# Performance work log

Measured on AMD Instinct MI355X. Metric: run time of the kernel, lower is better.

The kernel has to match this reference:

```python
import jax, jax.numpy as jnp
import numpy as np

# ---- MjCambrianEyeConfig constants ----
RES = (128, 128)              # sensor resolution (pixels)
SENSOR = (0.01, 0.01)         # sensor size Lx, Ly (meters)
APERTURE_OPEN = 0.5           # fraction of max aperture
FOCAL = 0.05                  # propagation distance z2 = config.focal[0] (meters)
WAVELENGTHS = (610e-9, 530e-9, 470e-9)  # R, G, B (meters)


def _rs_prop(u1, z, FX, FY, lmbda):
    # Rayleigh-Sommerfeld transfer-function propagation.
    k = 2.0 * np.pi / lmbda
    arg = 1.0 - (lmbda * FX) ** 2 - (lmbda * FY) ** 2  # (My, Mx)
    valid = jnp.sqrt(FX ** 2 + FY ** 2) < 1.0 / lmbda   # matches H_valid; arg>0 <=> valid
    H = jnp.where(valid, jnp.exp(1j * (k * z) * jnp.sqrt(jnp.where(arg > 0, arg, 0.0))), 0.0)
    U1 = jnp.fft.fft2(jnp.fft.fftshift(u1))
    U2 = jnp.fft.fftshift(H) * U1
    return jnp.fft.ifftshift(jnp.fft.ifft2(U2))


def _simple_psf(depth):
    Mx, My = RES[0] * 2, RES[1] * 2
    if Mx % 2 == 0:
        Mx += 1
    if My % 2 == 0:
        My += 1
    Lx, Ly = SENSOR
    dx, dy = Lx / Mx, Ly / My
    x1 = jnp.linspace(-Lx / 2.0, Lx / 2.0, Mx)
    y1 = jnp.linspace(-Ly / 2.0, Ly / 2.0, My)
    X1, Y1 = jnp.meshgrid(x1, y1)                         # (My, Mx)
    fx = jnp.linspace(-1.0 / (2.0 * dx), 1.0 / (2.0 * dx), Mx)
    fy = jnp.linspace(-1.0 / (2.0 * dy), 1.0 / (2.0 * dy), My)
    FX, FY = jnp.meshgrid(fx, fy)
    ap_radius = float(np.clip(APERTURE_OPEN, 0.0, 1.0)) * dx * (Mx // 2)
    R2 = X1 ** 2 + Y1 ** 2
    A = (jnp.sqrt(R2) / (ap_radius + 1e-7) <= 1.0).astype(jnp.float32)  # aperture mask
    z1 = jnp.mean(depth)
    psfs = []
    for lam in WAVELENGTHS:  # small fixed loop over 3 wavelengths
        k = 2.0 * np.pi / lam
        u = jnp.exp(1j * k * jnp.sqrt(R2 + z1 ** 2)) * A  # spherical wave at aperture
        u = _rs_prop(u, FOCAL, FX, FY, lam)
        psf = jnp.abs(u) ** 2
        psfs.append(psf / (jnp.sum(psf) + 1e-7))
    return jnp.stack(psfs, axis=-1).astype(jnp.float32)  # (My, Mx, 3)


def setup_inputs() -> dict:
    key = jax.random.key(0)
    k1, k2 = jax.random.split(key)
    image = jax.random.uniform(k1, (128, 128, 3), dtype=jnp.float32)
    depth = jax.random.uniform(k2, (128, 128), dtype=jnp.float32)
    return {"image": image, "depth": depth}


def reference(image, depth):
    psf = _simple_psf(depth)                       # (My, Mx, 3)
    lhs = jnp.transpose(image, (2, 0, 1))[None]    # (1, 3, H, W)
    rhs = jnp.transpose(psf, (2, 0, 1))[:, None]   # (3, 1, Kh, Kw)
    # Per-channel 'same' cross-correlation == torch conv2d per channel
    out = jax.lax.conv_general_dilated(lhs, rhs, window_strides=(1, 1), padding='SAME', feature_group_count=3)
    img = jnp.transpose(out[0], (1, 2, 0))         # (H, W, 3)
    return img, psf
```

## Files before the change

kernel.cpp:

```cpp
#include <hip/hip_runtime.h>
#include <math.h>

#define NN 257
#define NN2 66049
#define PROW 260
#define PCH (PROW * NN)
#define NRZ 17
#define FSW 288

#define SWG(f) (((((f) >> 2) ^ (((f) >> 5) & 7)) << 2))
#define SW(f) (SWG(f) | ((f) & 3))

static const double D_PI = 3.14159265358979323846;

__device__ __forceinline__ double lam_of(int c) {
    return c == 0 ? 610e-9 : (c == 1 ? 530e-9 : 470e-9);
}

__device__ __forceinline__ float2 phase_of(double rev) {
    rev -= floor(rev);
    float ang = (float)(2.0 * D_PI * rev);
    float sv, cv;
    __sincosf(ang, &sv, &cv);
    return make_float2(cv, sv);
}

__global__ __launch_bounds__(256) void k_prep(const float* __restrict__ depth, const float* __restrict__ img,
                                              double* zs, float* __restrict__ imgp, float2* __restrict__ twg) {
    if (blockIdx.x == 0) {
        __shared__ double s[256];
        double acc = 0.0;
        for (int i = threadIdx.x; i < 16384; i += 256) acc += (double)depth[i];
        s[threadIdx.x] = acc;
        __syncthreads();
        for (int o = 128; o > 0; o >>= 1) {
            if (threadIdx.x < o) s[threadIdx.x] += s[threadIdx.x + o];
            __syncthreads();
        }
        if (threadIdx.x == 0) {
            zs[0] = s[0] / 16384.0;
            zs[1] = 0.0; zs[2] = 0.0; zs[3] = 0.0;
        }
    } else if (blockIdx.x == 193) {
        int m = threadIdx.x;
        double th = 2.0 * D_PI * (double)m / 257.0;
        double sv, cv; sincos(th, &sv, &cv);
        twg[m] = make_float2((float)cv, (float)(-sv));
        if (m == 0) {
            th = 2.0 * D_PI * 256.0 / 257.0;
            sincos(th, &sv, &cv);
            twg[256] = make_float2((float)cv, (float)(-sv));
        }
    } else {
        int idx = (blockIdx.x - 1) * 256 + threadIdx.x;
        int c = idx / 16384;
        int r = idx & 16383;
        imgp[c * 16384 + r] = img[r * 3 + c];
    }
}

template <int SIGN, int MODE>
__global__ __launch_bounds__(256) void k_dft(const float2* __restrict__ in, float2* __restrict__ out,
                                             const float2* __restrict__ twg, const double* __restrict__ zs,
                                             float* __restrict__ raw, double* __restrict__ sums) {
    __shared__ float4 col[NN];
    __shared__ float2 twL[NN];
    __shared__ float4 sacc2[3][64][2];
    __shared__ float4 red[4];
    const int ah = blockIdx.x;
    const int by = blockIdx.y;
    const int c = blockIdx.z;
    int bc0, bc1;
    if (MODE == 0 || MODE == 3) {
        bc0 = (by < 64) ? 2 * by : 256;
        bc1 = (by < 64) ? bc0 + 1 : 256;
    } else if (MODE == 1) {
        bc0 = (by < 64) ? 2 * by : 128;
        bc1 = (by < 64) ? bc0 + 1 : 128;
    } else {
        bc0 = 2 * by;
        bc1 = (bc0 < 256) ? bc0 + 1 : 256;
    }
    const float dupf = (bc1 == bc0) ? 0.f : 1.f;
    const int tid = threadIdx.x;

    for (int t = tid; t < NN; t += 256) {
        twL[t] = twg[t];
        float2 v0, v1;
        if (MODE == 0) {
            int js = t + 129; if (js >= NN) js -= NN;
            const double step = 0.01 / 256.0;
            double yy = -0.005 + js * step;
            double z1 = zs[0];
            double lam = lam_of(c);
            const double ap = 0.5 * (0.01 / 257.0) * 128.0 + 1e-7;
            {
                int is = bc0 + 129; if (is >= NN) is -= NN;
                double x = -0.005 + is * step;
                double r2 = x * x + yy * yy;
                v0 = make_float2(0.f, 0.f);
                if (sqrt(r2) <= ap) v0 = phase_of(sqrt(r2 + z1 * z1) / lam);
            }
            {
                int is = bc1 + 129; if (is >= NN) is -= NN;
                double x = -0.005 + is * step;
                double r2 = x * x + yy * yy;
                v1 = make_float2(0.f, 0.f);
                if (sqrt(r2) <= ap) v1 = phase_of(sqrt(r2 + z1 * z1) / lam);
            }
        } else {
            v0 = in[(c * NN + t) * NN + bc0];
            v1 = in[(c * NN + t) * NN + bc1];
            if (MODE == 2) {
                int ps = t + 129; if (ps >= NN) ps -= NN;
                const double fstep = 25700.0 / 256.0;
                double fy = -12850.0 + ps * fstep;
                double lam = lam_of(c);
                double ilam2 = 1.0 / (lam * lam);
                double kzr = 0.05 / lam;
                {
                    int qs = bc0 + 129; if (qs >= NN) qs -= NN;
                    double fx = -12850.0 + qs * fstep;
                    double lfx = lam * fx, lfy = lam * fy;
                    double a2 = 1.0 - lfx * lfx - lfy * lfy;
                    float2 hh = make_float2(0.f, 0.f);
                    if (fx * fx + fy * fy < ilam2) hh = phase_of(kzr * sqrt(a2 > 0.0 ? a2 : 0.0));
                    v0 = make_float2(v0.x * hh.x - v0.y * hh.y, v0.x * hh.y + v0.y * hh.x);
                }
                {
                    int qs = bc1 + 129; if (qs >= NN) qs -= NN;
                    double fx = -12850.0 + qs * fstep;
                    double lfx = lam * fx, lfy = lam * fy;
                    double a2 = 1.0 - lfx * lfx - lfy * lfy;
                    float2 hh = make_float2(0.f, 0.f);
                    if (fx * fx + fy * fy < ilam2) hh = phase_of(kzr * sqrt(a2 > 0.0 ? a2 : 0.0));
                    v1 = make_float2(v1.x * hh.x - v1.y * hh.y, v1.x * hh.y + v1.y * hh.x);
                }
            }
        }
        col[t] = make_float4(v0.x, v0.y, v1.x, v1.y);
    }
    __syncthreads();

    const float invn4 = (float)(1.0 / ((double)NN2 * (double)NN2));
    const int q = tid >> 6;
    const int al = tid & 63;
    int aval[2];
    aval[0] = ah * 128 + al;
    aval[1] = aval[0] + 64;

    float cx[2][4], cy[2][4], wx[2], wy[2];
    #pragma unroll
    for (int aa = 0; aa < 2; ++aa) {
        #pragma unroll
        for (int m = 0; m < 4; ++m) {
            int sm = (aval[aa] * (q + 4 * m)) % 257;
            float2 tt = twL[sm];
            cx[aa][m] = tt.x; cy[aa][m] = -SIGN * tt.y;
        }
        float2 w16 = twL[(16 * aval[aa]) % 257];
        wx[aa] = w16.x; wy[aa] = -SIGN * w16.y;
    }

    float AX0[2] = {0.f, 0.f}, AY0[2] = {0.f, 0.f}, BX0[2] = {0.f, 0.f}, BY0[2] = {0.f, 0.f};
    float AX1[2] = {0.f, 0.f}, AY1[2] = {0.f, 0.f}, BX1[2] = {0.f, 0.f}, BY1[2] = {0.f, 0.f};

    for (int j = 0; j < 16; ++j) {
        const int tbase = q + 16 * j;
        #pragma unroll
        for (int m = 0; m < 4; ++m) {
            float4 v = col[tbase + 4 * m];
            #pragma unroll
            for (int aa = 0; aa < 2; ++aa) {
                float cxr = cx[aa][m], cyr = cy[aa][m];
                if (m < 2) {
                    AX0[aa] = fmaf(v.x, cxr, AX0[aa]); AX0[aa] = fmaf(-v.y, cyr, AX0[aa]);
                    AY0[aa] = fmaf(v.x, cyr, AY0[aa]); AY0[aa] = fmaf(v.y, cxr, AY0[aa]);
                    BX0[aa] = fmaf(v.z, cxr, BX0[aa]); BX0[aa] = fmaf(-v.w, cyr, BX0[aa]);
                    BY0[aa] = fmaf(v.z, cyr, BY0[aa]); BY0[aa] = fmaf(v.w, cxr, BY0[aa]);
                } else {
                    AX1[aa] = fmaf(v.x, cxr, AX1[aa]); AX1[aa] = fmaf(-v.y, cyr, AX1[aa]);
                    AY1[aa] = fmaf(v.x, cyr, AY1[aa]); AY1[aa] = fmaf(v.y, cxr, AY1[aa]);
                    BX1[aa] = fmaf(v.z, cxr, BX1[aa]); BX1[aa] = fmaf(-v.w, cyr, BX1[aa]);
                    BY1[aa] = fmaf(v.z, cyr, BY1[aa]); BY1[aa] = fmaf(v.w, cxr, BY1[aa]);
                }
                float nx = fmaf(cxr, wx[aa], -cyr * wy[aa]);
                float ny = fmaf(cxr, wy[aa], cyr * wx[aa]);
                cx[aa][m] = nx; cy[aa][m] = ny;
            }
        }
    }

    float ax0[2], ay0[2], ax1[2], ay1[2];
    #pragma unroll
    for (int aa = 0; aa < 2; ++aa) {
        ax0[aa] = AX0[aa] + AX1[aa]; ay0[aa] = AY0[aa] + AY1[aa];
        ax1[aa] = BX0[aa] + BX1[aa]; ay1[aa] = BY0[aa] + BY1[aa];
    }

    if (q == 0) {
        float4 v = col[256];
        #pragma unroll
        for (int aa = 0; aa < 2; ++aa) {
            float2 tb = twL[aval[aa]];
            float ex = tb.x, ey = SIGN * tb.y;
            ax0[aa] = fmaf(v.x, ex, ax0[aa]); ax0[aa] = fmaf(-v.y, ey, ax0[aa]);
            ay0[aa] = fmaf(v.x, ey, ay0[aa]); ay0[aa] = fmaf(v.y, ex, ay0[aa]);
            ax1[aa] = fmaf(v.z, ex, ax1[aa]); ax1[aa] = fmaf(-v.w, ey, ax1[aa]);
            ay1[aa] = fmaf(v.z, ey, ay1[aa]); ay1[aa] = fmaf(v.w, ex, ay1[aa]);
        }
    } else {
        #pragma unroll
        for (int aa = 0; aa < 2; ++aa)
            sacc2[q - 1][al][aa] = make_float4(ax0[aa], ay0[aa], ax1[aa], ay1[aa]);
    }
    __syncthreads();

    const bool mv0 = (MODE == 0) ? (bc0 <= 127) : (bc0 >= 1 && bc0 <= 128);
    const bool mv1 = ((MODE == 0) ? (bc1 <= 127) : (bc1 >= 1 && bc1 <= 128)) && (bc1 != bc0);
    const int bm0 = (MODE == 0) ? (255 - bc0) : (257 - bc0);
    const int bm1 = (MODE == 0) ? (255 - bc1) : (257 - bc1);
    const bool pm = (MODE == 3) && (bc0 <= 127);

    double sum_local = 0.0;
    if (q == 0) {
        #pragma unroll
        for (int aa = 0; aa < 2; ++aa) {
            #pragma unroll
            for (int r = 0; r < 3; ++r) {
                float4 b = sacc2[r][al][aa];
                ax0[aa] += b.x; ay0[aa] += b.y; ax1[aa] += b.z; ay1[aa] += b.w;
            }
            if (MODE < 3) {
                out[(c * NN + bc0) * NN + aval[aa]] = make_float2(ax0[aa], ay0[aa]);
                out[(c * NN + bc1) * NN + aval[aa]] = make_float2(ax1[aa], ay1[aa]);
                if (MODE < 2) {
                    const int a = aval[aa];
                    const int am = (a == 0) ? 0 : (257 - a);
                    if (mv0) {
                        int m = 2 * a + ((MODE == 1) ? 2 * bc0 : 0);
                        m %= 257;
                        float fx = twL[m].x, fy = -SIGN * twL[m].y;
                        out[(c * NN + bm0) * NN + am] =
                            make_float2(ax0[aa] * fx - ay0[aa] * fy, ax0[aa] * fy + ay0[aa] * fx);
                    }
                    if (mv1) {
                        int m = 2 * a + ((MODE == 1) ? 2 * bc1 : 0);
                        m %= 257;
                        float fx = twL[m].x, fy = -SIGN * twL[m].y;
                        out[(c * NN + bm1) * NN + am] =
                            make_float2(ax1[aa] * fx - ay1[aa] * fy, ax1[aa] * fy + ay1[aa] * fx);
                    }
                }
            } else {
                int jj0 = bc0 + 129; if (jj0 >= NN) jj0 -= NN;
                int jj1 = bc1 + 129; if (jj1 >= NN) jj1 -= NN;
                int ii = aval[aa] + 129; if (ii >= NN) ii -= NN;
                float m0 = fmaf(ax0[aa], ax0[aa], ay0[aa] * ay0[aa]) * invn4;
                float m1 = fmaf(ax1[aa], ax1[aa], ay1[aa] * ay1[aa]) * invn4;
                raw[c * PCH + jj0 * PROW + ii] = m0;
                raw[c * PCH + jj1 * PROW + ii] = m1;
                sum_local += (double)m0 + (double)(dupf * m1);
                if (pm) {
                    int im = 256 - ii;
                    raw[c * PCH + (256 - jj0) * PROW + im] = m0;
                    raw[c * PCH + (256 - jj1) * PROW + im] = m1;
                    sum_local += (double)m0 + (double)(dupf * m1);
                }
            }
        }
    }

    if (ah == (int)gridDim.x - 1) {
        float c_ = twL[tid].x, s_ = SIGN * twL[tid].y;
        float4 cv = col[tid];
        float tx0 = cv.x * c_ - cv.y * s_;
        float ty0 = cv.x * s_ + cv.y * c_;
        float tx1 = cv.z * c_ - cv.w * s_;
        float ty1 = cv.z * s_ + cv.w * c_;
        if (tid == 0) {
            c_ = twL[256].x; s_ = SIGN * twL[256].y;
            cv = col[256];
            tx0 += cv.x * c_ - cv.y * s_;
            ty0 += cv.x * s_ + cv.y * c_;
            tx1 += cv.z * c_ - cv.w * s_;
            ty1 += cv.z * s_ + cv.w * c_;
        }
        for (int o = 32; o > 0; o >>= 1) {
            tx0 += __shfl_down(tx0, o);
            ty0 += __shfl_down(ty0, o);
            tx1 += __shfl_down(tx1, o);
            ty1 += __shfl_down(ty1, o);
        }
        int wid = tid >> 6;
        if ((tid & 63) == 0) red[wid] = make_float4(tx0, ty0, tx1, ty1);
        __syncthreads();
        if (tid == 0) {
            float Xx0 = red[0].x + red[1].x + red[2].x + red[3].x;
            float Xy0 = red[0].y + red[1].y + red[2].y + red[3].y;
            float Xx1 = red[0].z + red[1].z + red[2].z + red[3].z;
            float Xy1 = red[0].w + red[1].w + red[2].w + red[3].w;
            if (MODE < 3) {
                out[(c * NN + bc0) * NN + 256] = make_float2(Xx0, Xy0);
                out[(c * NN + bc1) * NN + 256] = make_float2(Xx1, Xy1);
                if (MODE < 2) {
                    if (mv0) {
                        int m = 512 + ((MODE == 1) ? 2 * bc0 : 0);
                        m %= 257;
                        float fx = twL[m].x, fy = -SIGN * twL[m].y;
                        out[(c * NN + bm0) * NN + 1] = make_float2(Xx0 * fx - Xy0 * fy, Xx0 * fy + Xy0 * fx);
                    }
                    if (mv1) {
                        int m = 512 + ((MODE == 1) ? 2 * bc1 : 0);
                        m %= 257;
                        float fx = twL[m].x, fy = -SIGN * twL[m].y;
                        out[(c * NN + bm1) * NN + 1] = make_float2(Xx1 * fx - Xy1 * fy, Xx1 * fy + Xy1 * fx);
                    }
                }
            } else {
                int jj0 = bc0 + 129; if (jj0 >= NN) jj0 -= NN;
                int jj1 = bc1 + 129; if (jj1 >= NN) jj1 -= NN;
                float m0 = fmaf(Xx0, Xx0, Xy0 * Xy0) * invn4;
                float m1 = fmaf(Xx1, Xx1, Xy1 * Xy1) * invn4;
                raw[c * PCH + jj0 * PROW + 128] = m0;
                raw[c * PCH + jj1 * PROW + 128] = m1;
                sum_local += (double)m0 + (double)(dupf * m1);
                if (pm) {
                    raw[c * PCH + (256 - jj0) * PROW + 128] = m0;
                    raw[c * PCH + (256 - jj1) * PROW + 128] = m1;
                    sum_local += (double)m0 + (double)(dupf * m1);
                }
            }
        }
    }

    if (MODE == 3) {
        if (tid < 64) {
            double s = sum_local;
            for (int o = 32; o > 0; o >>= 1) s += __shfl_down(s, o);
            if (tid == 0) atomicAdd(&sums[c], s);
        }
    }
}

#define CM16(A, P, Q, iv)                                                                                   \
    A.x = fmaf(iv.x, Q.x, A.x); A.x = fmaf(iv.y, P.w, A.x); A.x = fmaf(iv.z, P.z, A.x); A.x = fmaf(iv.w, P.y, A.x); \
    A.y = fmaf(iv.x, Q.y, A.y); A.y = fmaf(iv.y, Q.x, A.y); A.y = fmaf(iv.z, P.w, A.y); A.y = fmaf(iv.w, P.z, A.y); \
    A.z = fmaf(iv.x, Q.z, A.z); A.z = fmaf(iv.y, Q.y, A.z); A.z = fmaf(iv.z, Q.x, A.z); A.z = fmaf(iv.w, P.w, A.z); \
    A.w = fmaf(iv.x, Q.w, A.w); A.w = fmaf(iv.y, Q.z, A.w); A.w = fmaf(iv.z, Q.y, A.w); A.w = fmaf(iv.w, Q.x, A.w);

__global__ __launch_bounds__(256) void k_conv(const float* __restrict__ imgp, const float* __restrict__ psf,
                                              float* __restrict__ part) {
    __shared__ float F[8][FSW];
    __shared__ float simg[15][132];
    __shared__ float sacc[3][4][260];
    const int yt = blockIdx.x;
    const int rz = blockIdx.y;
    const int c = blockIdx.z;
    const int y0 = yt * 8;
    const int r0 = 121 - y0 + 8 * rz;
    const int tid = threadIdx.x;
    const int tx = tid & 7;
    const int ty = (tid >> 3) & 7;
    const int rh = tid >> 6;
    const int x0 = 16 * tx;
    const int ulo = 8 * rz - 7;

    for (int g = tid; g < 8 * 65; g += 256) {
        int rr = g / 65, q = g - 65 * rr;
        const float* G = psf + c * PCH + (r0 + rr) * PROW + 4 * q;
        float4 A = *(const float4*)G;
        if (q < 64) {
            F[rr][SW(256 - 4 * q)] = A.x;
            F[rr][SW(255 - 4 * q)] = A.y;
            F[rr][SW(254 - 4 * q)] = A.z;
            F[rr][SW(253 - 4 * q)] = A.w;
        } else {
            F[rr][SW(0)] = A.x;
        }
    }
    for (int g = tid; g < 15 * 32; g += 256) {
        int rw = g >> 5, q = g & 31;
        int u = ulo + rw;
        float4 v = make_float4(0.f, 0.f, 0.f, 0.f);
        if (u >= 0 && u < 128) v = *(const float4*)(imgp + c * 16384 + u * 128 + 4 * q);
        *(float4*)&simg[rw][4 * q] = v;
    }
    __syncthreads();

    float4 A0 = make_float4(0.f, 0.f, 0.f, 0.f), A1 = A0, A2 = A0, A3 = A0;

    #pragma unroll
    for (int rr2 = 0; rr2 < 2; ++rr2) {
        const int rr = 2 * rh + rr2;
        const float* Fr = &F[rr][0];
        const float* I = &simg[ty + rr][0];
        float4 W0c = *(const float4*)(Fr + SWG(x0 + 128));
        float4 W1c = *(const float4*)(Fr + SWG(x0 + 132));
        float4 W2c = *(const float4*)(Fr + SWG(x0 + 136));
        float4 W3c = *(const float4*)(Fr + SWG(x0 + 140));
        #pragma unroll 2
        for (int vb = 0; vb < 128; vb += 4) {
            float4 Wm1 = *(const float4*)(Fr + SWG(x0 + 124 - vb));
            float4 iv = *(const float4*)(I + vb);
            CM16(A0, Wm1, W0c, iv)
            CM16(A1, W0c, W1c, iv)
            CM16(A2, W1c, W2c, iv)
            CM16(A3, W2c, W3c, iv)
            W3c = W2c; W2c = W1c; W1c = W0c; W0c = Wm1;
        }
    }

    if (rh != 0) {
        int s = tid & 63;
        *(float4*)&sacc[rh - 1][0][4 * s] = A0;
        *(float4*)&sacc[rh - 1][1][4 * s] = A1;
        *(float4*)&sacc[rh - 1][2][4 * s] = A2;
        *(float4*)&sacc[rh - 1][3][4 * s] = A3;
    }
    __syncthreads();
    if (rh == 0) {
        int s = tid;
        #pragma unroll
        for (int r = 0; r < 3; ++r) {
            float4 b0 = *(const float4*)&sacc[r][0][4 * s];
            float4 b1 = *(const float4*)&sacc[r][1][4 * s];
            float4 b2 = *(const float4*)&sacc[r][2][4 * s];
            float4 b3 = *(const float4*)&sacc[r][3][4 * s];
            A0.x += b0.x; A0.y += b0.y; A0.z += b0.z; A0.w += b0.w;
            A1.x += b1.x; A1.y += b1.y; A1.z += b1.z; A1.w += b1.w;
            A2.x += b2.x; A2.y += b2.y; A2.z += b2.z; A2.w += b2.w;
            A3.x += b3.x; A3.y += b3.y; A3.z += b3.z; A3.w += b3.w;
        }
        const int y = y0 + ty;
        float* dst = part + ((rz * 3 + c) * 128 + y) * 128 + x0;
        *(float4*)dst = A0;
        *(float4*)(dst + 4) = A1;
        *(float4*)(dst + 8) = A2;
        *(float4*)(dst + 12) = A3;
    }
}

__global__ __launch_bounds__(256) void k_final(const float* __restrict__ part, const float* __restrict__ raw,
                                               const double* __restrict__ zs, float* __restrict__ out) {
    int gid = blockIdx.x * 256 + threadIdx.x;
    if (gid < 49152) {
        int c = gid >> 14;
        int r = gid & 16383;
        float s = 0.f;
        #pragma unroll
        for (int rz = 0; rz < NRZ; ++rz) s += part[((rz * 3 + c) * 128 + (r >> 7)) * 128 + (r & 127)];
        float inv = (float)(1.0 / (zs[1 + c] + 1e-7));
        out[r * 3 + c] = s * inv;
    } else {
        int o = gid - 49152;
        if (o < 3 * NN2) {
            int idx = o / 3, c = o - 3 * idx;
            int j = idx / NN, i = idx - NN * j;
            float inv = (float)(1.0 / (zs[1 + c] + 1e-7));
            out[49152 + o] = raw[c * PCH + j * PROW + i] * inv;
        }
    }
}

extern "C" void kernel_launch(void* const* d_in, const int* in_sizes, int n_in,
                              void* d_out, int out_size, void* d_ws, size_t ws_size,
                              hipStream_t stream) {
    const float* img = (const float*)d_in[0];
    const float* depth = (const float*)d_in[1];
    float* out = (float*)d_out;

    char* ws = (char*)d_ws;
    double* zs = (double*)ws;
    float2* bufA = (float2*)(ws + 64);
    float2* bufB = bufA + 3 * NN2;
    float* raw = (float*)(bufB + 3 * NN2);
    float* imgp = raw + 3 * PCH;
    float2* twg = (float2*)(imgp + 3 * 16384);
    float* part = (float*)((char*)twg + 2176);

    k_prep<<<194, 256, 0, stream>>>(depth, img, zs, imgp, twg);
    k_dft<-1, 0><<<dim3(2, 65, 3), 256, 0, stream>>>(nullptr, bufA, twg, zs, nullptr, nullptr);
    k_dft<-1, 1><<<dim3(2, 65, 3), 256, 0, stream>>>(bufA, bufB, twg, zs, nullptr, nullptr);
    k_dft< 1, 2><<<dim3(1, 129, 3), 256, 0, stream>>>(bufB, bufA, twg, zs, nullptr, nullptr);
    k_dft< 1, 3><<<dim3(2, 65, 3), 256, 0, stream>>>(bufA, nullptr, twg, zs, raw, zs + 1);
    k_conv<<<dim3(16, NRZ, 3), 256, 0, stream>>>(imgp, raw, part);
    k_final<<<(49152 + 3 * NN2 + 255) / 256, 256, 0, stream>>>(part, raw, zs, out);
}
```

Baseline: 85.52 us.

## Fold prep kernel into DFT and conv kernels, remove one launch

Removes the separate prep kernel. Each DFT block now computes the twiddle table in-block with double-precision sincos. Every MODE 0 block recomputes the depth mean with its own reduction, and the first MODE 2 block zeroes the sum accumulators. The conv kernel reads the interleaved image directly with strided loads instead of using a pre-transposed planar copy. This saves one kernel launch and a small memory pass, at the cost of redundant depth reductions across 390 blocks and per-block sincos work.

```diff
diff --git a/kernel.cpp b/kernel.cpp
--- a/kernel.cpp
+++ b/kernel.cpp
@@ -25,43 +25,9 @@
     return make_float2(cv, sv);
 }
 
-__global__ __launch_bounds__(256) void k_prep(const float* __restrict__ depth, const float* __restrict__ img,
-                                              double* zs, float* __restrict__ imgp, float2* __restrict__ twg) {
-    if (blockIdx.x == 0) {
-        __shared__ double s[256];
-        double acc = 0.0;
-        for (int i = threadIdx.x; i < 16384; i += 256) acc += (double)depth[i];
-        s[threadIdx.x] = acc;
-        __syncthreads();
-        for (int o = 128; o > 0; o >>= 1) {
-            if (threadIdx.x < o) s[threadIdx.x] += s[threadIdx.x + o];
-            __syncthreads();
-        }
-        if (threadIdx.x == 0) {
-            zs[0] = s[0] / 16384.0;
-            zs[1] = 0.0; zs[2] = 0.0; zs[3] = 0.0;
-        }
-    } else if (blockIdx.x == 193) {
-        int m = threadIdx.x;
-        double th = 2.0 * D_PI * (double)m / 257.0;
-        double sv, cv; sincos(th, &sv, &cv);
-        twg[m] = make_float2((float)cv, (float)(-sv));
-        if (m == 0) {
-            th = 2.0 * D_PI * 256.0 / 257.0;
-            sincos(th, &sv, &cv);
-            twg[256] = make_float2((float)cv, (float)(-sv));
-        }
-    } else {
-        int idx = (blockIdx.x - 1) * 256 + threadIdx.x;
-        int c = idx / 16384;
-        int r = idx & 16383;
-        imgp[c * 16384 + r] = img[r * 3 + c];
-    }
-}
-
 template <int SIGN, int MODE>
 __global__ __launch_bounds__(256) void k_dft(const float2* __restrict__ in, float2* __restrict__ out,
-                                             const float2* __restrict__ twg, const double* __restrict__ zs,
+                                             const float* __restrict__ depth,
                                              float* __restrict__ raw, double* __restrict__ sums) {
     __shared__ float4 col[NN];
     __shared__ float2 twL[NN];
@@ -84,14 +50,37 @@
     const float dupf = (bc1 == bc0) ? 0.f : 1.f;
     const int tid = threadIdx.x;
 
+    if (MODE == 2) {
+        if (ah == 0 && by == 0 && tid == 0) sums[c] = 0.0;
+    }
+
     for (int t = tid; t < NN; t += 256) {
-        twL[t] = twg[t];
+        double th = 2.0 * D_PI * (double)t / 257.0;
+        double sv, cv; sincos(th, &sv, &cv);
+        twL[t] = make_float2((float)cv, (float)(-sv));
+    }
+
+    double z1 = 0.0;
+    if (MODE == 0) {
+        double* sred = (double*)sacc2;
+        double acc = 0.0;
+        for (int i = tid; i < 16384; i += 256) acc += (double)depth[i];
+        sred[tid] = acc;
+        __syncthreads();
+        for (int o = 128; o > 0; o >>= 1) {
+            if (tid < o) sred[tid] += sred[tid + o];
+            __syncthreads();
+        }
+        z1 = sred[0] / 16384.0;
+        __syncthreads();
+    }
+
+    for (int t = tid; t < NN; t += 256) {
         float2 v0, v1;
         if (MODE == 0) {
             int js = t + 129; if (js >= NN) js -= NN;
             const double step = 0.01 / 256.0;
             double yy = -0.005 + js * step;
-            double z1 = zs[0];
             double lam = lam_of(c);
             const double ap = 0.5 * (0.01 / 257.0) * 128.0 + 1e-7;
             {
@@ -349,7 +338,7 @@
     A.z = fmaf(iv.x, Q.z, A.z); A.z = fmaf(iv.y, Q.y, A.z); A.z = fmaf(iv.z, Q.x, A.z); A.z = fmaf(iv.w, P.w, A.z); \
     A.w = fmaf(iv.x, Q.w, A.w); A.w = fmaf(iv.y, Q.z, A.w); A.w = fmaf(iv.z, Q.y, A.w); A.w = fmaf(iv.w, Q.x, A.w);
 
-__global__ __launch_bounds__(256) void k_conv(const float* __restrict__ imgp, const float* __restrict__ psf,
+__global__ __launch_bounds__(256) void k_conv(const float* __restrict__ img, const float* __restrict__ psf,
                                               float* __restrict__ part) {
     __shared__ float F[8][FSW];
     __shared__ float simg[15][132];
@@ -383,7 +372,10 @@
         int rw = g >> 5, q = g & 31;
         int u = ulo + rw;
         float4 v = make_float4(0.f, 0.f, 0.f, 0.f);
-        if (u >= 0 && u < 128) v = *(const float4*)(imgp + c * 16384 + u * 128 + 4 * q);
+        if (u >= 0 && u < 128) {
+            const float* I = img + (u * 128 + 4 * q) * 3 + c;
+            v = make_float4(I[0], I[3], I[6], I[9]);
+        }
         *(float4*)&simg[rw][4 * q] = v;
     }
     __syncthreads();
@@ -442,7 +434,7 @@
 }
 
 __global__ __launch_bounds__(256) void k_final(const float* __restrict__ part, const float* __restrict__ raw,
-                                               const double* __restrict__ zs, float* __restrict__ out) {
+                                               const double* __restrict__ sums, float* __restrict__ out) {
     int gid = blockIdx.x * 256 + threadIdx.x;
     if (gid < 49152) {
         int c = gid >> 14;
@@ -450,14 +442,14 @@
         float s = 0.f;
         #pragma unroll
         for (int rz = 0; rz < NRZ; ++rz) s += part[((rz * 3 + c) * 128 + (r >> 7)) * 128 + (r & 127)];
-        float inv = (float)(1.0 / (zs[1 + c] + 1e-7));
+        float inv = (float)(1.0 / (sums[c] + 1e-7));
         out[r * 3 + c] = s * inv;
     } else {
         int o = gid - 49152;
         if (o < 3 * NN2) {
             int idx = o / 3, c = o - 3 * idx;
             int j = idx / NN, i = idx - NN * j;
-            float inv = (float)(1.0 / (zs[1 + c] + 1e-7));
+            float inv = (float)(1.0 / (sums[c] + 1e-7));
             out[49152 + o] = raw[c * PCH + j * PROW + i] * inv;
         }
     }
@@ -471,19 +463,16 @@
     float* out = (float*)d_out;
 
     char* ws = (char*)d_ws;
-    double* zs = (double*)ws;
+    double* zsums = (double*)ws;
     float2* bufA = (float2*)(ws + 64);
     float2* bufB = bufA + 3 * NN2;
     float* raw = (float*)(bufB + 3 * NN2);
-    float* imgp = raw + 3 * PCH;
-    float2* twg = (float2*)(imgp + 3 * 16384);
-    float* part = (float*)((char*)twg + 2176);
-
-    k_prep<<<194, 256, 0, stream>>>(depth, img, zs, imgp, twg);
-    k_dft<-1, 0><<<dim3(2, 65, 3), 256, 0, stream>>>(nullptr, bufA, twg, zs, nullptr, nullptr);
-    k_dft<-1, 1><<<dim3(2, 65, 3), 256, 0, stream>>>(bufA, bufB, twg, zs, nullptr, nullptr);
-    k_dft< 1, 2><<<dim3(1, 129, 3), 256, 0, stream>>>(bufB, bufA, twg, zs, nullptr, nullptr);
-    k_dft< 1, 3><<<dim3(2, 65, 3), 256, 0, stream>>>(bufA, nullptr, twg, zs, raw, zs + 1);
-    k_conv<<<dim3(16, NRZ, 3), 256, 0, stream>>>(imgp, raw, part);
-    k_final<<<(49152 + 3 * NN2 + 255) / 256, 256, 0, stream>>>(part, raw, zs, out);
-}
+    float* part = raw + 3 * PCH;
+
+    k_dft<-1, 0><<<dim3(2, 65, 3), 256, 0, stream>>>(nullptr, bufA, depth, nullptr, nullptr);
+    k_dft<-1, 1><<<dim3(2, 65, 3), 256, 0, stream>>>(bufA, bufB, nullptr, nullptr, nullptr);
+    k_dft< 1, 2><<<dim3(1, 129, 3), 256, 0, stream>>>(bufB, bufA, nullptr, nullptr, zsums);
+    k_dft< 1, 3><<<dim3(2, 65, 3), 256, 0, stream>>>(bufA, nullptr, nullptr, raw, zsums);
+    k_conv<<<dim3(16, NRZ, 3), 256, 0, stream>>>(img, raw, part);
+    k_final<<<(49152 + 3 * NN2 + 255) / 256, 256, 0, stream>>>(part, raw, zsums, out);
+}
```

After: 83.07 us. 2.9% less time.
